# Optimization experiments

Measured on AMD Instinct MI355X. Metric: run time of the kernel, lower is better.

## Reference

```python
import jax, jax.numpy as jnp
import numpy as np

B, S, D, H = 4, 2048, 512, 8
DH = D // H  # head dim = 64
NEG = -1000000.0


def setup_inputs() -> dict:
    key = jax.random.key(0)
    ks = jax.random.split(key, 13)
    s = 1.0 / np.sqrt(D)
    return {
        "Q": jax.random.normal(ks[0], (B, S, D), jnp.float32),
        "K": jax.random.normal(ks[1], (B, S, D), jnp.float32),
        "V": jax.random.normal(ks[2], (B, S, D), jnp.float32),
        "Wq": jax.random.normal(ks[3], (D, D), jnp.float32) * s,
        "bq": jnp.zeros((D,), jnp.float32),
        "Wk": jax.random.normal(ks[4], (D, D), jnp.float32) * s,
        "bk": jnp.zeros((D,), jnp.float32),
        "Wv": jax.random.normal(ks[5], (D, D), jnp.float32) * s,
        "bv": jnp.zeros((D,), jnp.float32),
        "Wo": jax.random.normal(ks[6], (D, D), jnp.float32) * s,
        "bo": jnp.zeros((D,), jnp.float32),
        "masked": jax.random.randint(ks[7], (B,), 1, S + 1, jnp.int64),
    }


def _heads(x):
    # [B,S,D] -> [B,H,S,DH]
    return x.reshape(B, S, H, DH).transpose(0, 2, 1, 3)


def reference(Q, K, V, Wq, bq, Wk, bk, Wv, bv, Wo, bo, masked):
    q = _heads(Q @ Wq.T + bq)
    k = _heads(K @ Wk.T + bk)
    v = _heads(V @ Wv.T + bv)
    scores = jnp.einsum("bhqd,bhkd->bhqk", q, k) / jnp.sqrt(jnp.asarray(DH, q.dtype))
    # valid-length key mask, per batch (same for every head and query row)
    key_mask = jnp.arange(S)[None, None, None, :] < masked[:, None, None, None]
    scores = jnp.where(key_mask, scores, jnp.asarray(NEG, scores.dtype))
    weights = jax.nn.softmax(scores, axis=-1)
    out = jnp.einsum("bhqk,bhkd->bhqd", weights, v)  # [B,H,S,DH]
    out = out.transpose(0, 2, 1, 3).reshape(B, S, D)
    return out @ Wo.T + bo
```

## Files before the change

### kernel.cpp

```cpp
#include <hip/hip_runtime.h>
#include <stdint.h>


typedef __attribute__((ext_vector_type(8))) short short8;
typedef __attribute__((ext_vector_type(4))) short short4v;
typedef __attribute__((ext_vector_type(4))) float f32x4;
typedef __attribute__((ext_vector_type(4))) unsigned short u16x4;

#define MFMA16(a, b, c) __builtin_amdgcn_mfma_f32_16x16x32_bf16(a, b, c, 0, 0, 0)

#define SCALE_LOG2 0.18033688011112042f
#define FIXED_M    32.0f
#define MASKED_E2  -200.0f

__device__ __forceinline__ unsigned short f2bf(float f) {
    unsigned int x = __float_as_uint(f);
    unsigned int r = (x + 0x7fffu + ((x >> 16) & 1u)) >> 16;
    return (unsigned short)r;
}
__device__ __forceinline__ short8 load8(const unsigned short* p) {
    return *reinterpret_cast<const short8*>(p);
}
__device__ __forceinline__ void gload_lds16(const unsigned short* g, unsigned short* l) {
    __builtin_amdgcn_global_load_lds(
        (const __attribute__((address_space(1))) unsigned int*)g,
        (__attribute__((address_space(3))) unsigned int*)l, 16, 0, 0);
}

__global__ __launch_bounds__(256)
void convert_bf16(const float4* __restrict__ Q, const float4* __restrict__ K,
                  const float4* __restrict__ V, const float4* __restrict__ Wq,
                  const float4* __restrict__ Wk, const float4* __restrict__ Wv,
                  const float4* __restrict__ Wo, u16x4* __restrict__ dst)
{
    const int n = 3407872;
    for (int i = blockIdx.x * 256 + threadIdx.x; i < n; i += gridDim.x * 256) {
        const float4* src; int off;
        if      (i < 1048576) { src = Q;  off = i; }
        else if (i < 2097152) { src = K;  off = i - 1048576; }
        else if (i < 3145728) { src = V;  off = i - 2097152; }
        else if (i < 3211264) { src = Wq; off = i - 3145728; }
        else if (i < 3276800) { src = Wk; off = i - 3211264; }
        else if (i < 3342336) { src = Wv; off = i - 3276800; }
        else                  { src = Wo; off = i - 3342336; }
        const float4 v = src[off];
        u16x4 r;
        r[0] = f2bf(v.x); r[1] = f2bf(v.y); r[2] = f2bf(v.z); r[3] = f2bf(v.w);
        dst[i] = r;
    }
}

__global__ __launch_bounds__(256)
void gemm_bf(const unsigned short* __restrict__ Aall,
             const unsigned short* __restrict__ Wall,
             const float* __restrict__ b0, const float* __restrict__ b1,
             const float* __restrict__ b2,
             void* __restrict__ outall, int out_mode)
{
    __shared__ unsigned short As[128 * 64];
    __shared__ unsigned short Bs[128 * 64];

    const int z = blockIdx.y;
    const unsigned short* A = Aall + (long)z * 4194304;
    const unsigned short* W = Wall + z * 262144;
    const float* bias = (z == 0) ? b0 : (z == 1) ? b1 : b2;
    void* out = (out_mode == 0)
        ? (void*)((unsigned short*)outall + (long)z * 4194304) : outall;

    const int f    = blockIdx.x;
    const int xcd  = f & 7;
    const int slot = f >> 3;
    const int col0 = (slot & 3) * 128;
    const int row0 = ((slot >> 2) * 8 + xcd) * 128;

    const int tid  = threadIdx.x;
    const int lane = tid & 63;
    const int w    = tid >> 6;
    const int quad = lane >> 4;
    const int nlow = lane & 15;
    const int wm   = w >> 1, wn = w & 1;

    const unsigned short* ag[4];
    const unsigned short* wg[4];
    unsigned short *la[4], *lb[4];
#pragma unroll
    for (int i = 0; i < 4; i++) {
        const int s = i * 256 + tid;
        const int r = s >> 3, kcl = s & 7;
        const int kg = kcl ^ (r & 7);
        ag[i] = A + (long)(row0 + r) * 512 + kg * 8;
        wg[i] = W + (long)(col0 + r) * 512 + kg * 8;
        const int ldso = i * 2048 + ((tid >> 6) << 9);
        la[i] = As + ldso;
        lb[i] = Bs + ldso;
    }

    f32x4 acc[4][4];
#pragma unroll
    for (int t = 0; t < 4; t++)
#pragma unroll
        for (int g = 0; g < 4; g++) acc[t][g] = (f32x4){0.f, 0.f, 0.f, 0.f};

    for (int k0 = 0; k0 < 512; k0 += 64) {
#pragma unroll
        for (int i = 0; i < 4; i++) {
            gload_lds16(ag[i] + k0, la[i]);
            gload_lds16(wg[i] + k0, lb[i]);
        }
        __syncthreads();

        short8 af[4][2], bf[4][2];
#pragma unroll
        for (int t = 0; t < 4; t++) {
            const int rowa = wm * 64 + t * 16 + nlow;
            const int rowb = wn * 64 + t * 16 + nlow;
#pragma unroll
            for (int kc = 0; kc < 2; kc++) {
                const int c = (kc * 4 + quad) ^ (nlow & 7);
                af[t][kc] = load8(&As[(rowa * 8 + c) * 8]);
                bf[t][kc] = load8(&Bs[(rowb * 8 + c) * 8]);
            }
        }
#pragma unroll
        for (int kc = 0; kc < 2; kc++)
#pragma unroll
            for (int t = 0; t < 4; t++)
#pragma unroll
                for (int g = 0; g < 4; g++)
                    acc[t][g] = MFMA16(af[t][kc], bf[g][kc], acc[t][g]);
        __syncthreads();
    }

#pragma unroll
    for (int g = 0; g < 4; g++) {
        const int j = col0 + wn * 64 + g * 16 + nlow;
        const float bj = bias[j];
#pragma unroll
        for (int t = 0; t < 4; t++) {
#pragma unroll
            for (int r = 0; r < 4; r++) {
                const int i = row0 + wm * 64 + t * 16 + quad * 4 + r;
                const float v = acc[t][g][r] + bj;
                if (out_mode == 0) {
                    const int b = i >> 11, s = i & 2047;
                    const int h = j >> 6, dh = j & 63;
                    ((unsigned short*)out)[(((b * 8 + h) * 2048) + s) * 64 + dh] = f2bf(v);
                } else {
                    ((float*)out)[(long)i * 512 + j] = v;
                }
            }
        }
    }
}

__device__ __forceinline__ int ks_idx(int key, int dchunk) {
    return key * 64 + ((dchunk ^ (key & 7)) << 3);
}
__device__ __forceinline__ int vt_idx(int key, int dh) {
    return dh * 64 + ((((key >> 3) ^ (dh & 7) ^ ((dh >> 3) & 7)) << 3) + (key & 7));
}
__device__ __forceinline__ int ps_idx(int q, int key) {
    return q * 64 + ((((key >> 3) ^ (q & 7)) << 3) + (key & 7));
}

__global__ __launch_bounds__(256, 4)
void attn_kernel(const unsigned short* __restrict__ qp,
                 const unsigned short* __restrict__ kp,
                 const unsigned short* __restrict__ vp,
                 const void* __restrict__ masked,
                 unsigned short* __restrict__ out)
{
    __shared__ unsigned short Ks[2][4096];
    __shared__ unsigned short Vt[2][4096];
    __shared__ unsigned short Ps[4][1024];

    const int tid  = threadIdx.x;
    const int lane = tid & 63;
    const int w    = tid >> 6;
    const int quad = lane >> 4;
    const int nlow = lane & 15;

    const int f  = blockIdx.x;
    const int h  = f & 7;
    const int qb = (f >> 3) & 31;
    const int b  = f >> 8;
    const int q0 = qb * 64 + w * 16;
    const long base = ((long)(b * 8 + h)) * 2048 * 64;

    const long long first = *reinterpret_cast<const long long*>(masked);
    int kmax;
    if ((first >> 32) != 0) kmax = reinterpret_cast<const int*>(masked)[b];
    else                    kmax = (int)reinterpret_cast<const long long*>(masked)[b];
    kmax = min(max(kmax, 1), 2048);
    const int nkt = (kmax + 63) >> 6;

    const unsigned short* qrow = qp + base + (long)(q0 + nlow) * 64;
    const short8 aq0 = load8(qrow + quad * 8);
    const short8 aq1 = load8(qrow + 32 + quad * 8);

    short8 ones;
#pragma unroll
    for (int j = 0; j < 8; j++) ones[j] = (short)0x3F80;

    f32x4 o_acc[4], lacc;
#pragma unroll
    for (int vb = 0; vb < 4; vb++) o_acc[vb] = (f32x4){0.f, 0.f, 0.f, 0.f};
    lacc = (f32x4){0.f, 0.f, 0.f, 0.f};

    const int kr0 = tid >> 3;
    const int kr1 = 32 + kr0;
    const unsigned short* kg0 = kp + base + (long)kr0 * 64 + (((tid & 7) ^ (kr0 & 7)) << 3);
    const unsigned short* kg1 = kp + base + (long)kr1 * 64 + (((tid & 7) ^ (kr1 & 7)) << 3);
    const int kd0 = (w << 9);
    const int kd1 = 2048 + (w << 9);
    const int vk0 = tid >> 3;
    const int vk1 = 32 + vk0;
    const int vd0 = (tid & 7) << 3;
    const unsigned short* vg0 = vp + base + (long)vk0 * 64 + vd0;
    const unsigned short* vg1 = vp + base + (long)vk1 * 64 + vd0;

    gload_lds16(kg0, &Ks[0][kd0]);
    gload_lds16(kg1, &Ks[0][kd1]);
    {
        short8 v0 = load8(vg0);
        short8 v1 = load8(vg1);
#pragma unroll
        for (int j = 0; j < 8; j++) {
            Vt[0][vt_idx(vk0, vd0 + j)] = (unsigned short)v0[j];
            Vt[0][vt_idx(vk1, vd0 + j)] = (unsigned short)v1[j];
        }
    }
    __syncthreads();

    unsigned short* Psw = Ps[w];
    int cur = 0;
    short8 vv0, vv1;

    for (int kt = 0; kt < nkt; kt++) {
        const int k0 = kt * 64;
        const bool more = (kt + 1 < nkt);
        if (more) {
            const long off = (long)(k0 + 64) * 64;
            gload_lds16(kg0 + off, &Ks[cur ^ 1][kd0]);
            gload_lds16(kg1 + off, &Ks[cur ^ 1][kd1]);
            vv0 = load8(vg0 + off);
            vv1 = load8(vg1 + off);
        }
        const unsigned short* Ksc = Ks[cur];
        const unsigned short* Vtc = Vt[cur];

        f32x4 sacc[4];
#pragma unroll
        for (int kb = 0; kb < 4; kb++) sacc[kb] = (f32x4){0.f, 0.f, 0.f, 0.f};
        __builtin_amdgcn_s_setprio(1);
#pragma unroll
        for (int kb = 0; kb < 4; kb++) {
            const int key = kb * 16 + nlow;
            short8 bk0 = load8(Ksc + ks_idx(key, quad));
            short8 bk1 = load8(Ksc + ks_idx(key, 4 + quad));
            sacc[kb] = MFMA16(aq0, bk0, sacc[kb]);
            sacc[kb] = MFMA16(aq1, bk1, sacc[kb]);
        }
        __builtin_amdgcn_s_setprio(0);

#pragma unroll
        for (int kb = 0; kb < 4; kb++) {
            const bool valid = (k0 + kb * 16 + nlow) < kmax;
#pragma unroll
            for (int r = 0; r < 4; r++) {
                const int q = quad * 4 + r;
                const float e = valid ? fmaf(sacc[kb][r], SCALE_LOG2, -FIXED_M)
                                      : MASKED_E2;
                Psw[ps_idx(q, kb * 16 + nlow)] = f2bf(exp2f(e));
            }
        }
        __threadfence_block();

        __builtin_amdgcn_s_setprio(1);
#pragma unroll
        for (int h2 = 0; h2 < 2; h2++) {
            const int g = h2 * 4 + quad;
            short8 ap = load8(Psw + ps_idx(nlow, g << 3));
            lacc = MFMA16(ap, ones, lacc);
#pragma unroll
            for (int vb = 0; vb < 4; vb++) {
                short8 bv = load8(Vtc + vt_idx(g << 3, vb * 16 + nlow));
                o_acc[vb] = MFMA16(ap, bv, o_acc[vb]);
            }
        }
        __builtin_amdgcn_s_setprio(0);

        if (more) {
            unsigned short* Vtn = Vt[cur ^ 1];
#pragma unroll
            for (int j = 0; j < 8; j++) {
                Vtn[vt_idx(vk0, vd0 + j)] = (unsigned short)vv0[j];
                Vtn[vt_idx(vk1, vd0 + j)] = (unsigned short)vv1[j];
            }
        }
        __syncthreads();
        cur ^= 1;
    }

    float inv_l[4];
#pragma unroll
    for (int r = 0; r < 4; r++) inv_l[r] = 1.0f / lacc[r];
#pragma unroll
    for (int vb = 0; vb < 4; vb++) {
#pragma unroll
        for (int r = 0; r < 4; r++) {
            const int s   = q0 + quad * 4 + r;
            const int col = h * 64 + vb * 16 + nlow;
            out[(long)(b * 2048 + s) * 512 + col] = f2bf(o_acc[vb][r] * inv_l[r]);
        }
    }
}

extern "C" void kernel_launch(void* const* d_in, const int* in_sizes, int n_in,
                              void* d_out, int out_size, void* d_ws, size_t ws_size,
                              hipStream_t stream)
{
    const float4* Q  = (const float4*)d_in[0];
    const float4* K  = (const float4*)d_in[1];
    const float4* V  = (const float4*)d_in[2];
    const float4* Wq = (const float4*)d_in[3];
    const float*  bq = (const float*)d_in[4];
    const float4* Wk = (const float4*)d_in[5];
    const float*  bk = (const float*)d_in[6];
    const float4* Wv = (const float4*)d_in[7];
    const float*  bv = (const float*)d_in[8];
    const float4* Wo = (const float4*)d_in[9];
    const float*  bo = (const float*)d_in[10];
    const void*   masked = d_in[11];

    unsigned short* ws16 = (unsigned short*)d_ws;
    unsigned short* QKVb = ws16;
    unsigned short* Wb   = ws16 + 12582912;
    unsigned short* qp   = ws16 + 13631488;
    unsigned short* kp   = qp + 4194304;
    unsigned short* vp   = kp + 4194304;
    unsigned short* ao   = ws16;

    convert_bf16<<<2048, 256, 0, stream>>>(Q, K, V, Wq, Wk, Wv, Wo, (u16x4*)ws16);
    gemm_bf<<<dim3(256, 3), 256, 0, stream>>>(QKVb, Wb, bq, bk, bv, qp, 0);
    attn_kernel<<<dim3(1024), 256, 0, stream>>>(qp, kp, vp, masked, ao);
    gemm_bf<<<dim3(256, 1), 256, 0, stream>>>(ao, Wb + 3 * 262144, bo, bo, bo,
                                              d_out, 1);
}
```

Measured before the change: 175.8 us.

## Fuse fp32-to-bf16 conversion of Q/K/V into the projection GEMM

Stops converting the large Q, K and V activations to bf16 in a separate pass. A new QKV GEMM streams fp32 tiles straight into LDS and converts them to bf16 in registers with packed convert instructions before the MFMAs, so only the weights are still pre-converted. This removes one full write and re-read of the activations through global memory. In exchange the A tile in LDS is twice as large and each k-step loads twice the bytes, which may lower occupancy.

```diff
diff --git a/kernel.cpp b/kernel.cpp
--- a/kernel.cpp
+++ b/kernel.cpp
@@ -3,7 +3,6 @@
 
 
 typedef __attribute__((ext_vector_type(8))) short short8;
-typedef __attribute__((ext_vector_type(4))) short short4v;
 typedef __attribute__((ext_vector_type(4))) float f32x4;
 typedef __attribute__((ext_vector_type(4))) unsigned short u16x4;
 
@@ -18,6 +17,11 @@
     unsigned int r = (x + 0x7fffu + ((x >> 16) & 1u)) >> 16;
     return (unsigned short)r;
 }
+__device__ __forceinline__ unsigned int cvt_pk_bf16(float lo, float hi) {
+    unsigned int r;
+    asm("v_cvt_pk_bf16_f32 %0, %1, %2" : "=v"(r) : "v"(lo), "v"(hi));
+    return r;
+}
 __device__ __forceinline__ short8 load8(const unsigned short* p) {
     return *reinterpret_cast<const short8*>(p);
 }
@@ -28,25 +32,131 @@
 }
 
 __global__ __launch_bounds__(256)
-void convert_bf16(const float4* __restrict__ Q, const float4* __restrict__ K,
-                  const float4* __restrict__ V, const float4* __restrict__ Wq,
-                  const float4* __restrict__ Wk, const float4* __restrict__ Wv,
-                  const float4* __restrict__ Wo, u16x4* __restrict__ dst)
+void convert_w(const float4* __restrict__ Wq, const float4* __restrict__ Wk,
+               const float4* __restrict__ Wv, const float4* __restrict__ Wo,
+               u16x4* __restrict__ dst)
 {
-    const int n = 3407872;
+    const int n = 262144;
     for (int i = blockIdx.x * 256 + threadIdx.x; i < n; i += gridDim.x * 256) {
         const float4* src; int off;
-        if      (i < 1048576) { src = Q;  off = i; }
-        else if (i < 2097152) { src = K;  off = i - 1048576; }
-        else if (i < 3145728) { src = V;  off = i - 2097152; }
-        else if (i < 3211264) { src = Wq; off = i - 3145728; }
-        else if (i < 3276800) { src = Wk; off = i - 3211264; }
-        else if (i < 3342336) { src = Wv; off = i - 3276800; }
-        else                  { src = Wo; off = i - 3342336; }
+        if      (i < 65536)  { src = Wq; off = i; }
+        else if (i < 131072) { src = Wk; off = i - 65536; }
+        else if (i < 196608) { src = Wv; off = i - 131072; }
+        else                 { src = Wo; off = i - 196608; }
         const float4 v = src[off];
         u16x4 r;
         r[0] = f2bf(v.x); r[1] = f2bf(v.y); r[2] = f2bf(v.z); r[3] = f2bf(v.w);
         dst[i] = r;
+    }
+}
+
+__global__ __launch_bounds__(256, 3)
+void gemm_qkv_f32(const float* __restrict__ Qf, const float* __restrict__ Kf,
+                  const float* __restrict__ Vf,
+                  const unsigned short* __restrict__ Wall,
+                  const float* __restrict__ b0, const float* __restrict__ b1,
+                  const float* __restrict__ b2,
+                  unsigned short* __restrict__ outall)
+{
+    __shared__ float          Asf[128 * 64];
+    __shared__ unsigned short Bs[128 * 64];
+
+    const int z = blockIdx.y;
+    const float* A    = (z == 0) ? Qf : (z == 1) ? Kf : Vf;
+    const unsigned short* W = Wall + z * 262144;
+    const float* bias = (z == 0) ? b0 : (z == 1) ? b1 : b2;
+    unsigned short* out = outall + (long)z * 4194304;
+
+    const int f    = blockIdx.x;
+    const int xcd  = f & 7;
+    const int slot = f >> 3;
+    const int col0 = (slot & 3) * 128;
+    const int row0 = ((slot >> 2) * 8 + xcd) * 128;
+
+    const int tid  = threadIdx.x;
+    const int lane = tid & 63;
+    const int w    = tid >> 6;
+    const int quad = lane >> 4;
+    const int nlow = lane & 15;
+    const int wm   = w >> 1, wn = w & 1;
+
+    const int arow = tid >> 4;
+    const int ag   = (tid & 15) ^ (arow & 15);
+    const float* abase = A + (long)(row0 + arow) * 512 + ag * 4;
+    unsigned short* adst = (unsigned short*)(Asf + tid * 4);
+
+    const unsigned short* wg[4];
+    unsigned short* lb[4];
+#pragma unroll
+    for (int i = 0; i < 4; i++) {
+        const int s = i * 256 + tid;
+        const int r = s >> 3, kcl = s & 7;
+        const int kg = kcl ^ (r & 7);
+        wg[i] = W + (long)(col0 + r) * 512 + kg * 8;
+        lb[i] = Bs + i * 2048 + (w << 9);
+    }
+
+    f32x4 acc[4][4];
+#pragma unroll
+    for (int t = 0; t < 4; t++)
+#pragma unroll
+        for (int g = 0; g < 4; g++) acc[t][g] = (f32x4){0.f, 0.f, 0.f, 0.f};
+
+    for (int k0 = 0; k0 < 512; k0 += 64) {
+#pragma unroll
+        for (int i = 0; i < 8; i++)
+            gload_lds16((const unsigned short*)(abase + k0 + i * 8192),
+                        adst + i * 2048);
+#pragma unroll
+        for (int i = 0; i < 4; i++)
+            gload_lds16(wg[i] + k0, lb[i]);
+        __syncthreads();
+
+        short8 af[4][2], bfr[4][2];
+#pragma unroll
+        for (int t = 0; t < 4; t++) {
+            const int rowa = wm * 64 + t * 16 + nlow;
+            const int rowb = wn * 64 + t * 16 + nlow;
+#pragma unroll
+            for (int kc = 0; kc < 2; kc++) {
+                const int c0 = (kc * 8 + quad * 2)     ^ (rowa & 15);
+                const int c1 = (kc * 8 + quad * 2 + 1) ^ (rowa & 15);
+                const float4 fa0 = *reinterpret_cast<const float4*>(&Asf[(rowa * 16 + c0) * 4]);
+                const float4 fa1 = *reinterpret_cast<const float4*>(&Asf[(rowa * 16 + c1) * 4]);
+                uint4 u;
+                u.x = cvt_pk_bf16(fa0.x, fa0.y);
+                u.y = cvt_pk_bf16(fa0.z, fa0.w);
+                u.z = cvt_pk_bf16(fa1.x, fa1.y);
+                u.w = cvt_pk_bf16(fa1.z, fa1.w);
+                af[t][kc] = __builtin_bit_cast(short8, u);
+                const int cb = (kc * 4 + quad) ^ (nlow & 7);
+                bfr[t][kc] = load8(&Bs[(rowb * 8 + cb) * 8]);
+            }
+        }
+#pragma unroll
+        for (int kc = 0; kc < 2; kc++)
+#pragma unroll
+            for (int t = 0; t < 4; t++)
+#pragma unroll
+                for (int g = 0; g < 4; g++)
+                    acc[t][g] = MFMA16(af[t][kc], bfr[g][kc], acc[t][g]);
+        __syncthreads();
+    }
+
+#pragma unroll
+    for (int g = 0; g < 4; g++) {
+        const int j = col0 + wn * 64 + g * 16 + nlow;
+        const float bj = bias[j];
+        const int h = j >> 6, dh = j & 63;
+#pragma unroll
+        for (int t = 0; t < 4; t++) {
+#pragma unroll
+            for (int r = 0; r < 4; r++) {
+                const int i = row0 + wm * 64 + t * 16 + quad * 4 + r;
+                const int b = i >> 11, s = i & 2047;
+                out[(((b * 8 + h) * 2048) + s) * 64 + dh] = f2bf(acc[t][g][r] + bj);
+            }
+        }
     }
 }
 
@@ -320,9 +430,9 @@
                               void* d_out, int out_size, void* d_ws, size_t ws_size,
                               hipStream_t stream)
 {
-    const float4* Q  = (const float4*)d_in[0];
-    const float4* K  = (const float4*)d_in[1];
-    const float4* V  = (const float4*)d_in[2];
+    const float* Q  = (const float*)d_in[0];
+    const float* K  = (const float*)d_in[1];
+    const float* V  = (const float*)d_in[2];
     const float4* Wq = (const float4*)d_in[3];
     const float*  bq = (const float*)d_in[4];
     const float4* Wk = (const float4*)d_in[5];
@@ -334,15 +444,14 @@
     const void*   masked = d_in[11];
 
     unsigned short* ws16 = (unsigned short*)d_ws;
-    unsigned short* QKVb = ws16;
-    unsigned short* Wb   = ws16 + 12582912;
-    unsigned short* qp   = ws16 + 13631488;
-    unsigned short* kp   = qp + 4194304;
-    unsigned short* vp   = kp + 4194304;
-    unsigned short* ao   = ws16;
-
-    convert_bf16<<<2048, 256, 0, stream>>>(Q, K, V, Wq, Wk, Wv, Wo, (u16x4*)ws16);
-    gemm_bf<<<dim3(256, 3), 256, 0, stream>>>(QKVb, Wb, bq, bk, bv, qp, 0);
+    unsigned short* Wb = ws16;
+    unsigned short* qp = ws16 + 1048576;
+    unsigned short* kp = qp + 4194304;
+    unsigned short* vp = kp + 4194304;
+    unsigned short* ao = vp + 4194304;
+
+    convert_w<<<256, 256, 0, stream>>>(Wq, Wk, Wv, Wo, (u16x4*)Wb);
+    gemm_qkv_f32<<<dim3(256, 3), 256, 0, stream>>>(Q, K, V, Wb, bq, bk, bv, qp);
     attn_kernel<<<dim3(1024), 256, 0, stream>>>(qp, kp, vp, masked, ao);
     gemm_bf<<<dim3(256, 1), 256, 0, stream>>>(ao, Wb + 3 * 262144, bo, bo, bo,
                                               d_out, 1);
```

New measurement: 177.0 us. About the same (+0.6%).
